# Performance work log

Measured on AMD Instinct MI355X. Metric: run time of the kernel, lower is better.

## Reference

```python
import jax, jax.numpy as jnp
import numpy as np
from jax.scipy.special import logsumexp

DIM_N, DIM_E, DIM_U = 64, 128, 64
MID, A = 32, 16
N_PER, B = 12, 128  # 128 fully-connected graphs of 12 nodes


def _lin_params(k, fin, fout):
    k1, k2 = jax.random.split(k)
    lim = 1.0 / np.sqrt(fin)
    W = jax.random.uniform(k1, (fin, fout), minval=-lim, maxval=lim)
    b = jax.random.uniform(k2, (fout,), minval=-lim, maxval=lim)
    return W, b


def setup_inputs() -> dict:
    key = jax.random.key(0)
    ks = jax.random.split(key, 12)
    # fully connected directed graph (no self loops), per component
    s, d = np.meshgrid(np.arange(N_PER), np.arange(N_PER), indexing='ij')
    m = s != d
    s1, d1 = s[m].astype(np.int64), d[m].astype(np.int64)
    Epg = s1.size  # 132
    M = np.zeros((N_PER, N_PER), np.int64)
    M[s1, d1] = np.arange(Epg)
    rev1 = M[d1, s1]
    noff = (np.arange(B, dtype=np.int64) * N_PER)[:, None]
    eoff = (np.arange(B, dtype=np.int64) * Epg)[:, None]
    src = jnp.asarray((s1[None] + noff).reshape(-1))
    dst = jnp.asarray((d1[None] + noff).reshape(-1))
    idx_revs = jnp.asarray((rev1[None] + eoff).reshape(-1))
    E, Nt = B * Epg, B * N_PER
    edge_feats = jax.random.normal(ks[0], (E, DIM_E))
    node_feats = jax.random.normal(ks[1], (Nt, DIM_N))
    graph_feats = jax.random.normal(ks[2], (B, DIM_U))
    edge_feat_reflected = edge_feats[idx_revs]
    u = jax.random.uniform(ks[3], (E, 2), minval=1e-6, maxval=1.0)
    gumbel_noise = -jnp.log(-jnp.log(u))
    W_jf, b_jf = _lin_params(ks[4], DIM_E + DIM_U, A * MID)
    W_if, b_if = _lin_params(ks[5], DIM_N + DIM_U, A)
    W_ju, b_ju = _lin_params(ks[6], DIM_E + DIM_U, A * MID)
    W_iu, b_iu = _lin_params(ks[7], DIM_N + DIM_U, A)
    W_fl, b_fl = _lin_params(ks[8], DIM_E + DIM_U, MID)
    W_cls, b_cls = _lin_params(ks[9], MID, 2)
    return dict(edge_feats=edge_feats, node_feats=node_feats, graph_feats=graph_feats,
                edge_feat_reflected=edge_feat_reflected, src=src, dst=dst, idx_revs=idx_revs,
                gumbel_noise=gumbel_noise, W_jf=W_jf, b_jf=b_jf, W_if=W_if, b_if=b_if,
                W_ju=W_ju, b_ju=b_ju, W_iu=W_iu, b_iu=b_iu, W_fl=W_fl, b_fl=b_fl,
                W_cls=W_cls, b_cls=b_cls)


def reference(edge_feats, node_feats, graph_feats, edge_feat_reflected, src, dst, idx_revs,
              gumbel_noise, W_jf, b_jf, W_if, b_if, W_ju, b_ju, W_iu, b_iu,
              W_fl, b_fl, W_cls, b_cls):
    Bn = graph_feats.shape[0]
    Nt = node_feats.shape[0]
    E = edge_feats.shape[0]
    npg = Nt // Bn          # nodes per graph == number of BP iterations
    epg = E // Bn
    a = b_if.shape[0]       # num_acts
    mid = W_cls.shape[0]    # mid_pair

    # broadcast graph-level features to edges / nodes
    u_e = jnp.repeat(graph_feats, epg, axis=0)   # [E, du]
    u_n = jnp.repeat(graph_feats, npg, axis=0)   # [Nt, du]

    xe = jnp.concatenate([edge_feats, u_e], axis=-1)
    xer = jnp.concatenate([edge_feat_reflected, u_e], axis=-1)
    xn = jnp.concatenate([node_feats, u_n], axis=-1)

    indiv_factor = xn @ W_if + b_if      # [Nt, A]
    indiv_util = xn @ W_iu + b_iu        # [Nt, A]

    fc = (xe @ W_jf + b_jf).reshape(E, a, mid)
    fcr = (xer @ W_jf + b_jf).reshape(E, a, mid)
    factor_vals = jnp.einsum('eam,ebm->eab', fc, fcr)   # [E, A, A]
    uc = (xe @ W_ju + b_ju).reshape(E, a, mid)
    ucr = (xer @ W_ju + b_ju).reshape(E, a, mid)
    util_vals = jnp.einsum('eam,ebm->eab', uc, ucr)     # [E, A, A]

    # hard gumbel-softmax edge gating; noise shared with reverse edge
    flag_repr = (xe @ W_fl + b_fl) * (xer @ W_fl + b_fl)
    logits = flag_repr @ W_cls + b_cls                  # [E, 2]
    eid = jnp.arange(E)
    noise = gumbel_noise[jnp.minimum(eid, idx_revs)]
    y_soft = jax.nn.softmax(logits + noise, axis=-1)
    y_hard = jax.nn.one_hot(jnp.argmax(y_soft, axis=-1), 2, dtype=y_soft.dtype)
    flags = y_soft + jax.lax.stop_gradient(y_hard - y_soft)
    flag0 = flags[:, 0][:, None]                        # [E, 1]

    fvT = factor_vals.transpose(0, 2, 1)
    uvT = util_vals.transpose(0, 2, 1)
    if_src, if_dst = indiv_factor[src], indiv_factor[dst]
    iu_src, iu_dst = indiv_util[src], indiv_util[dst]

    def step(carry, _):
        mm_n, um_n, msg_e, rmsg_e, umsg_e, rumsg_e = carry
        agg = mm_n[src] - rmsg_e + if_src                      # [E, A]
        m = factor_vals + agg[:, None, :]                      # [E, A, A]
        m_sum = jax.nn.log_softmax(logsumexp(m, axis=-1), axis=-1)
        new_msg = m_sum * flag0
        agg_rev = mm_n[dst] - msg_e + if_dst
        m_rev = fvT + agg_rev[:, None, :]
        m_rev_sum = jax.nn.log_softmax(logsumexp(m_rev, axis=-1), axis=-1)
        new_rmsg = m_rev_sum * flag0
        util = um_n[src] - rumsg_e + iu_src
        new_umsg = ((util_vals + util[:, None, :]) * jax.nn.softmax(m, axis=-1)).sum(-1) * flag0
        rev_util = um_n[dst] - umsg_e + iu_dst
        new_rumsg = ((uvT + rev_util[:, None, :]) * jax.nn.softmax(m_rev, axis=-1)).sum(-1) * flag0
        new_mm_n = jax.ops.segment_sum(new_msg, dst, num_segments=Nt)
        new_um_n = jax.ops.segment_sum(new_umsg, dst, num_segments=Nt)
        return (new_mm_n, new_um_n, new_msg, new_rmsg, new_umsg, new_rumsg), None

    zn = jnp.zeros((Nt, a), edge_feats.dtype)
    ze = jnp.zeros((E, a), edge_feats.dtype)
    carry0 = (zn, zn, ze, ze, ze, ze)
    (mm_n, um_n, _, _, _, _), _ = jax.lax.scan(step, carry0, None, length=npg)

    node0 = jnp.arange(Bn) * npg
    return (um_n + indiv_util)[node0]   # [B, A]
```

## Files before the change

kernel.cpp:

```cpp
#include <hip/hip_runtime.h>
#include <hip/hip_bf16.h>

typedef unsigned short ushort_t;
typedef __bf16 bf16x8 __attribute__((ext_vector_type(8)));
typedef float f32x4 __attribute__((ext_vector_type(4)));

#define E_TOT 16896
#define NT    1536
#define BGR   128
#define NPG   12
#define EPG   132
#define KD    192
#define KD2   576
#define NJ    512
#define NCAN  8448

#if defined(__has_builtin)
#  if __has_builtin(__builtin_amdgcn_global_load_lds)
#    define HAS_GLL 1
#  else
#    define HAS_GLL 0
#  endif
#else
#  define HAS_GLL 0
#endif

#if HAS_GLL
__device__ __forceinline__ void gll16(const ushort_t* g, ushort_t* s) {
    __builtin_amdgcn_global_load_lds(
        (const __attribute__((address_space(1))) unsigned int*)g,
        (__attribute__((address_space(3))) unsigned int*)s, 16, 0, 0);
}
#endif

__device__ __forceinline__ float b2f(ushort_t u) {
    union { float f; unsigned int i; } c; c.i = ((unsigned int)u) << 16; return c.f;
}
__device__ __forceinline__ ushort_t f2b(float f) {
    union { float f; unsigned int i; } c; c.f = f;
    unsigned int i = c.i;
    unsigned int r = (i + 0x7FFFu + ((i >> 16) & 1u)) >> 16;
    return (ushort_t)r;
}
__device__ __forceinline__ int rev_local(int i) {
    int s = i / 11;
    int p = i - 11 * s;
    int d = p + (p >= s ? 1 : 0);
    return d * 11 + (s < d ? s : s - 1);
}

__global__ __launch_bounds__(256) void prep_kernel(
    const float* __restrict__ Wjf, const float* __restrict__ Wju,
    const float* __restrict__ ef,  const float* __restrict__ gf,
    const float* __restrict__ nf,
    const float* __restrict__ Wif, const float* __restrict__ bif,
    const float* __restrict__ Wiu, const float* __restrict__ biu,
    ushort_t* __restrict__ WtJFs, ushort_t* __restrict__ WtJUs,
    ushort_t* __restrict__ XeS,
    float* __restrict__ IFF, float* __restrict__ IUU)
{
    __shared__ float Ws[128 * 32];
    __shared__ float xr[8][128];
    const int T1 = NJ * KD;
    const int NBE = (T1 + E_TOT * KD) / 256;
    if (blockIdx.x < (unsigned)NBE) {
        int idx = blockIdx.x * 256 + threadIdx.x;
        if (idx < T1) {
            int n = idx / KD, k = idx - n * KD;
            float wf = Wjf[k * NJ + n];
            ushort_t hf = f2b(wf);
            WtJFs[n * KD2 + k]       = hf;
            WtJFs[n * KD2 + 192 + k] = hf;
            WtJFs[n * KD2 + 384 + k] = f2b(wf - b2f(hf));
            float wu = Wju[k * NJ + n];
            ushort_t hu = f2b(wu);
            WtJUs[n * KD2 + k]       = hu;
            WtJUs[n * KD2 + 192 + k] = hu;
            WtJUs[n * KD2 + 384 + k] = f2b(wu - b2f(hu));
            return;
        }
        idx -= T1;
        int e = idx / KD, k = idx - e * KD;
        float x = (k < 128) ? ef[(size_t)e * 128 + k] : gf[(e / EPG) * 64 + (k - 128)];
        ushort_t h = f2b(x);
        XeS[(size_t)e * KD2 + k]       = h;
        XeS[(size_t)e * KD2 + 192 + k] = f2b(x - b2f(h));
        XeS[(size_t)e * KD2 + 384 + k] = h;
        return;
    }
    int tid = threadIdx.x;
    int n0 = (blockIdx.x - NBE) * 8;
    for (int i = tid; i < 128 * 32; i += 256) {
        int k = i >> 5, j = i & 31;
        Ws[i] = (j < 16) ? Wif[k * 16 + j] : Wiu[k * 16 + (j - 16)];
    }
    for (int i = tid; i < 8 * 128; i += 256) {
        int slot = i >> 7, k = i & 127;
        int n = n0 + slot;
        xr[slot][k] = (k < 64) ? nf[(size_t)n * 64 + k] : gf[(n / NPG) * 64 + (k - 64)];
    }
    __syncthreads();
    int slot = tid >> 5, j = tid & 31;
    float acc = (j < 16) ? bif[j] : biu[j - 16];
#pragma unroll 8
    for (int k = 0; k < 128; ++k) acc += xr[slot][k] * Ws[k * 32 + j];
    int n = n0 + slot;
    if (j < 16) IFF[n * 16 + j] = acc;
    else        IUU[n * 16 + (j - 16)] = acc;
}

__global__ __launch_bounds__(256) void gemm_kernel(
    const ushort_t* __restrict__ X,
    const ushort_t* __restrict__ Wt0, const ushort_t* __restrict__ Wt1,
    const float* __restrict__ b0, const float* __restrict__ b1,
    float* __restrict__ Hbase)
{
    __shared__ ushort_t As[2][128][32];
    __shared__ ushort_t Bs[2][2][128][32];
    int tid = threadIdx.x, lane = tid & 63, w = tid >> 6;
    int m0 = blockIdx.y * 128, n0 = blockIdx.x * 128;
    int wm = (w >> 1) * 64, wn = (w & 1) * 64;
    int r = lane & 15, q = lane >> 4;
    f32x4 acc[2][4][4] = {};

    int sr = w * 32 + (lane >> 2);
    int sc = (lane & 3) * 8;
    const ushort_t* xg0 = X   + (size_t)(m0 + sr)      * KD2 + sc;
    const ushort_t* xg1 = X   + (size_t)(m0 + sr + 16) * KD2 + sc;
    const ushort_t* w0g0 = Wt0 + (size_t)(n0 + sr)      * KD2 + sc;
    const ushort_t* w0g1 = Wt0 + (size_t)(n0 + sr + 16) * KD2 + sc;
    const ushort_t* w1g0 = Wt1 + (size_t)(n0 + sr)      * KD2 + sc;
    const ushort_t* w1g1 = Wt1 + (size_t)(n0 + sr + 16) * KD2 + sc;

#if HAS_GLL
    auto stage = [&](int p, int kk) {
        gll16(xg0 + kk,  &As[p][w * 32][0]);
        gll16(xg1 + kk,  &As[p][w * 32 + 16][0]);
        gll16(w0g0 + kk, &Bs[p][0][w * 32][0]);
        gll16(w0g1 + kk, &Bs[p][0][w * 32 + 16][0]);
        gll16(w1g0 + kk, &Bs[p][1][w * 32][0]);
        gll16(w1g1 + kk, &Bs[p][1][w * 32 + 16][0]);
    };
#else
    auto stage = [&](int p, int kk) {
        uint4 a0 = *(const uint4*)(xg0 + kk);
        uint4 a1 = *(const uint4*)(xg1 + kk);
        uint4 c0 = *(const uint4*)(w0g0 + kk);
        uint4 c1 = *(const uint4*)(w0g1 + kk);
        uint4 d0 = *(const uint4*)(w1g0 + kk);
        uint4 d1 = *(const uint4*)(w1g1 + kk);
        *(uint4*)&As[p][sr][sc]         = a0;
        *(uint4*)&As[p][sr + 16][sc]    = a1;
        *(uint4*)&Bs[p][0][sr][sc]      = c0;
        *(uint4*)&Bs[p][0][sr + 16][sc] = c1;
        *(uint4*)&Bs[p][1][sr][sc]      = d0;
        *(uint4*)&Bs[p][1][sr + 16][sc] = d1;
    };
#endif

    stage(0, 0);
    int cur = 0;
    for (int kk = 0; kk < KD2; kk += 32) {
        __syncthreads();
        if (kk + 32 < KD2) stage(cur ^ 1, kk + 32);
        bf16x8 af[4];
#pragma unroll
        for (int mi = 0; mi < 4; ++mi)
            af[mi] = *(const bf16x8*)&As[cur][wm + mi * 16 + r][q * 8];
#pragma unroll
        for (int z = 0; z < 2; ++z) {
            bf16x8 bf[4];
#pragma unroll
            for (int ni = 0; ni < 4; ++ni)
                bf[ni] = *(const bf16x8*)&Bs[cur][z][wn + ni * 16 + r][q * 8];
#pragma unroll
            for (int mi = 0; mi < 4; ++mi)
#pragma unroll
                for (int ni = 0; ni < 4; ++ni)
                    acc[z][mi][ni] = __builtin_amdgcn_mfma_f32_16x16x32_bf16(
                        af[mi], bf[ni], acc[z][mi][ni], 0, 0, 0);
        }
        cur ^= 1;
    }
#pragma unroll
    for (int z = 0; z < 2; ++z) {
        float* H = Hbase + (size_t)z * E_TOT * NJ;
        const float* bias = z ? b1 : b0;
#pragma unroll
        for (int ni = 0; ni < 4; ++ni) {
            int col = n0 + wn + ni * 16 + r;
            float bvf = bias[col];
#pragma unroll
            for (int mi = 0; mi < 4; ++mi) {
                int rowb = m0 + wm + mi * 16 + q * 4;
                float* dst = H + (size_t)rowb * NJ + col;
#pragma unroll
                for (int rr = 0; rr < 4; ++rr)
                    dst[(size_t)rr * NJ] = acc[z][mi][ni][rr] + bvf;
            }
        }
    }
}

__global__ __launch_bounds__(256) void pair_kernel(
    const float* __restrict__ Hbase, float* __restrict__ Obase)
{
    __shared__ float sA[4][16][36];
    __shared__ float sB[4][16][36];
    __shared__ float sC[4][16][20];
    const float* H = Hbase + (size_t)blockIdx.y * E_TOT * NJ;
    float* OutV = Obase + (size_t)blockIdx.y * E_TOT * 256;
    int tid = threadIdx.x, w = tid >> 6, lane = tid & 63;
    int c = blockIdx.x * 4 + w;
    int gg = c / 66, cl = c - gg * 66;
    int s = 0;
    while (cl >= 11 - s) { cl -= 11 - s; ++s; }
    int d = s + 1 + cl;
    int e  = gg * EPG + s * 11 + (d - 1);
    int re = gg * EPG + d * 11 + s;
    const float* hA = H + (size_t)e * NJ;
    const float* hB = H + (size_t)re * NJ;
    int a = lane >> 2, mseg = (lane & 3) * 8;
    float4 va0 = *(const float4*)(hA + a * 32 + mseg);
    float4 va1 = *(const float4*)(hA + a * 32 + mseg + 4);
    float4 vb0 = *(const float4*)(hB + a * 32 + mseg);
    float4 vb1 = *(const float4*)(hB + a * 32 + mseg + 4);
    *(float4*)&sA[w][a][mseg]     = va0;
    *(float4*)&sA[w][a][mseg + 4] = va1;
    *(float4*)&sB[w][a][mseg]     = vb0;
    *(float4*)&sB[w][a][mseg + 4] = vb1;
    __syncthreads();

    int b = lane & 15, a0 = (lane >> 4) * 4;
    float4 ac0 = {0,0,0,0}, ac1 = {0,0,0,0}, ac2 = {0,0,0,0}, ac3 = {0,0,0,0};
#pragma unroll
    for (int m4 = 0; m4 < 8; ++m4) {
        float4 vb = *(const float4*)&sB[w][b][m4 * 4];
        float4 x0 = *(const float4*)&sA[w][a0 + 0][m4 * 4];
        float4 x1 = *(const float4*)&sA[w][a0 + 1][m4 * 4];
        float4 x2 = *(const float4*)&sA[w][a0 + 2][m4 * 4];
        float4 x3 = *(const float4*)&sA[w][a0 + 3][m4 * 4];
        ac0.x += x0.x * vb.x; ac0.y += x0.y * vb.y; ac0.z += x0.z * vb.z; ac0.w += x0.w * vb.w;
        ac1.x += x1.x * vb.x; ac1.y += x1.y * vb.y; ac1.z += x1.z * vb.z; ac1.w += x1.w * vb.w;
        ac2.x += x2.x * vb.x; ac2.y += x2.y * vb.y; ac2.z += x2.z * vb.z; ac2.w += x2.w * vb.w;
        ac3.x += x3.x * vb.x; ac3.y += x3.y * vb.y; ac3.z += x3.z * vb.z; ac3.w += x3.w * vb.w;
    }
    float v0 = ac0.x + ac0.y + ac0.z + ac0.w;
    float v1 = ac1.x + ac1.y + ac1.z + ac1.w;
    float v2 = ac2.x + ac2.y + ac2.z + ac2.w;
    float v3 = ac3.x + ac3.y + ac3.z + ac3.w;
    float* oe = OutV + (size_t)e * 256;
    oe[(a0 + 0) * 16 + b] = v0;
    oe[(a0 + 1) * 16 + b] = v1;
    oe[(a0 + 2) * 16 + b] = v2;
    oe[(a0 + 3) * 16 + b] = v3;
    sC[w][b][a0 + 0] = v0;
    sC[w][b][a0 + 1] = v1;
    sC[w][b][a0 + 2] = v2;
    sC[w][b][a0 + 3] = v3;
    __syncthreads();
    int rr = lane >> 2, cc = (lane & 3) * 4;
    float4 t4 = { sC[w][rr][cc], sC[w][rr][cc + 1], sC[w][rr][cc + 2], sC[w][rr][cc + 3] };
    *(float4*)(OutV + (size_t)re * 256 + lane * 4) = t4;
}

__global__ __launch_bounds__(256) void hfl_kernel(
    const float* __restrict__ ef, const float* __restrict__ gf,
    const float* __restrict__ Wfl, const float* __restrict__ bfl,
    float* __restrict__ HFL)
{
    __shared__ float Ws[KD][32];
    __shared__ float xr[64][KD];
    int tid = threadIdx.x;
    int e0 = blockIdx.x * 64;
    for (int i = tid; i < KD * 32; i += 256) Ws[i >> 5][i & 31] = Wfl[i];
    for (int i4 = tid; i4 < 64 * 48; i4 += 256) {
        int slot = i4 / 48, kq = i4 - slot * 48;
        int e = e0 + slot;
        float4 v;
        if (kq < 32) v = *(const float4*)&ef[(size_t)e * 128 + kq * 4];
        else         v = *(const float4*)&gf[(e / EPG) * 64 + (kq - 32) * 4];
        *(float4*)&xr[slot][kq * 4] = v;
    }
    __syncthreads();
    int j = tid & 31, es = tid >> 5;
    float acc[8];
#pragma unroll
    for (int i = 0; i < 8; ++i) acc[i] = bfl[j];
    for (int k = 0; k < KD; k += 4) {
        float w0 = Ws[k][j], w1 = Ws[k + 1][j], w2 = Ws[k + 2][j], w3 = Ws[k + 3][j];
#pragma unroll
        for (int i = 0; i < 8; ++i) {
            float4 x4 = *(const float4*)&xr[es + 8 * i][k];
            acc[i] += x4.x * w0; acc[i] += x4.y * w1;
            acc[i] += x4.z * w2; acc[i] += x4.w * w3;
        }
    }
#pragma unroll
    for (int i = 0; i < 8; ++i)
        HFL[(size_t)(e0 + es + 8 * i) * 32 + j] = acc[i];
}

__global__ __launch_bounds__(704, 3) void bp_kernel(
    const float* __restrict__ FV, const float* __restrict__ UV,
    const float* __restrict__ HFL, const float* __restrict__ Wcls,
    const float* __restrict__ bcls, const float* __restrict__ gum,
    const float* __restrict__ IFF, const float* __restrict__ IUU,
    float* __restrict__ out)
{
    int g = blockIdx.x, tid = threadIdx.x;
    __shared__ float msg[2][EPG][16];
    __shared__ float umsg[2][EPG][16];
    __shared__ float Asum[NPG][16], Usum[NPG][16];
    __shared__ float iffs[NPG][16], iuus[NPG][16];
    __shared__ float fls[EPG];

    for (int i = tid; i < 2 * EPG * 16; i += 704) {
        (&msg[0][0][0])[i] = 0.f;
        (&umsg[0][0][0])[i] = 0.f;
    }
    if (tid < NPG * 16) {
        float fi = IFF[g * NPG * 16 + tid];
        float ui = IUU[g * NPG * 16 + tid];
        (&iffs[0][0])[tid] = fi; (&iuus[0][0])[tid] = ui;
        (&Asum[0][0])[tid] = fi; (&Usum[0][0])[tid] = ui;
    }
    if (tid < EPG) {
        int el = tid, rel = rev_local(el);
        int e = g * EPG + el, re = g * EPG + rel;
        float l0 = bcls[0], l1 = bcls[1];
        const float* ha = HFL + (size_t)e * 32;
        const float* hb = HFL + (size_t)re * 32;
#pragma unroll
        for (int j = 0; j < 32; ++j) {
            float pp = ha[j] * hb[j];
            l0 += pp * Wcls[j * 2 + 0];
            l1 += pp * Wcls[j * 2 + 1];
        }
        int mn = min(e, re);
        l0 += gum[(size_t)mn * 2 + 0];
        l1 += gum[(size_t)mn * 2 + 1];
        fls[el] = (l0 >= l1) ? 1.0f : 0.0f;
    }

    int w44 = tid >> 4, a = tid & 15;
    int sidx[3], ridx[3], eidx[3];
    float fv[3][16], uv[3][16], fle[3];
    const float* fvg = FV + (size_t)g * EPG * 256;
    const float* uvg = UV + (size_t)g * EPG * 256;
#pragma unroll
    for (int j = 0; j < 3; ++j) {
        int e = j * 44 + w44;
        eidx[j] = e;
        sidx[j] = e / 11;
        ridx[j] = rev_local(e);
        const float* fr = fvg + (size_t)e * 256 + a * 16;
        const float* ur = uvg + (size_t)e * 256 + a * 16;
#pragma unroll
        for (int qq = 0; qq < 4; ++qq) {
            float4 f4 = *(const float4*)(fr + qq * 4);
            float4 u4 = *(const float4*)(ur + qq * 4);
            fv[j][qq * 4 + 0] = f4.x; fv[j][qq * 4 + 1] = f4.y;
            fv[j][qq * 4 + 2] = f4.z; fv[j][qq * 4 + 3] = f4.w;
            uv[j][qq * 4 + 0] = u4.x; uv[j][qq * 4 + 1] = u4.y;
            uv[j][qq * 4 + 2] = u4.z; uv[j][qq * 4 + 3] = u4.w;
        }
    }
    __syncthreads();
#pragma unroll
    for (int j = 0; j < 3; ++j) fle[j] = fls[eidx[j]];

    int cur = 0;
    for (int it = 0; it < NPG; ++it) {
        int nxt = cur ^ 1;
#pragma unroll
        for (int j = 0; j < 3; ++j) {
            int e = eidx[j], s = sidx[j], re = ridx[j];
            float t_m[16], t_u[16];
#pragma unroll
            for (int qq = 0; qq < 4; ++qq) {
                float4 av  = *(const float4*)&Asum[s][qq * 4];
                float4 mv  = *(const float4*)&msg[cur][re][qq * 4];
                float4 usv = *(const float4*)&Usum[s][qq * 4];
                float4 umv = *(const float4*)&umsg[cur][re][qq * 4];
                t_m[qq * 4 + 0] = fv[j][qq * 4 + 0] + (av.x - mv.x);
                t_m[qq * 4 + 1] = fv[j][qq * 4 + 1] + (av.y - mv.y);
                t_m[qq * 4 + 2] = fv[j][qq * 4 + 2] + (av.z - mv.z);
                t_m[qq * 4 + 3] = fv[j][qq * 4 + 3] + (av.w - mv.w);
                t_u[qq * 4 + 0] = uv[j][qq * 4 + 0] + (usv.x - umv.x);
                t_u[qq * 4 + 1] = uv[j][qq * 4 + 1] + (usv.y - umv.y);
                t_u[qq * 4 + 2] = uv[j][qq * 4 + 2] + (usv.z - umv.z);
                t_u[qq * 4 + 3] = uv[j][qq * 4 + 3] + (usv.w - umv.w);
            }
            float mx = t_m[0];
#pragma unroll
            for (int b = 1; b < 16; ++b) mx = fmaxf(mx, t_m[b]);
            float S = 0.f, num = 0.f;
#pragma unroll
            for (int b = 0; b < 16; ++b) {
                float ev = __expf(t_m[b] - mx);
                S += ev;
                num += t_u[b] * ev;
            }
            float lse = mx + __logf(S);
            float unv = num / S;
            float M2 = lse;
            M2 = fmaxf(M2, __shfl_xor(M2, 1));
            M2 = fmaxf(M2, __shfl_xor(M2, 2));
            M2 = fmaxf(M2, __shfl_xor(M2, 4));
            M2 = fmaxf(M2, __shfl_xor(M2, 8));
            float se = __expf(lse - M2);
            se += __shfl_xor(se, 1);
            se += __shfl_xor(se, 2);
            se += __shfl_xor(se, 4);
            se += __shfl_xor(se, 8);
            float LSE = M2 + __logf(se);
            msg[nxt][e][a] = (lse - LSE) * fle[j];
            umsg[nxt][e][a] = unv * fle[j];
        }
        __syncthreads();
        if (tid < NPG * 16) {
            int n = tid >> 4, aa = tid & 15;
            float sm = 0.f, su = 0.f;
#pragma unroll
            for (int s = 0; s < NPG; ++s) {
                if (s == n) continue;
                int le = s * 11 + (n < s ? n : n - 1);
                sm += msg[nxt][le][aa];
                su += umsg[nxt][le][aa];
            }
            Asum[n][aa] = sm + iffs[n][aa];
            Usum[n][aa] = su + iuus[n][aa];
        }
        __syncthreads();
        cur = nxt;
    }
    if (tid < 16) {
        out[g * 16 + tid] = Usum[0][tid];
    }
}

extern "C" void kernel_launch(void* const* d_in, const int* in_sizes, int n_in,
                              void* d_out, int out_size, void* d_ws, size_t ws_size,
                              hipStream_t stream) {
    const float* edge_feats  = (const float*)d_in[0];
    const float* node_feats  = (const float*)d_in[1];
    const float* graph_feats = (const float*)d_in[2];
    const float* gumbel      = (const float*)d_in[7];
    const float* W_jf        = (const float*)d_in[8];
    const float* b_jf        = (const float*)d_in[9];
    const float* W_if        = (const float*)d_in[10];
    const float* b_if        = (const float*)d_in[11];
    const float* W_ju        = (const float*)d_in[12];
    const float* b_ju        = (const float*)d_in[13];
    const float* W_iu        = (const float*)d_in[14];
    const float* b_iu        = (const float*)d_in[15];
    const float* W_fl        = (const float*)d_in[16];
    const float* b_fl        = (const float*)d_in[17];
    const float* W_cls       = (const float*)d_in[18];
    const float* b_cls       = (const float*)d_in[19];
    float* out = (float*)d_out;
    (void)in_sizes; (void)n_in; (void)out_size; (void)ws_size;

    size_t off = 0;
    char* base = (char*)d_ws;
    auto alloc = [&](size_t bytes) {
        void* p = base + off;
        off += (bytes + 255) & ~(size_t)255;
        return p;
    };
    ushort_t* XeS   = (ushort_t*)alloc((size_t)E_TOT * KD2 * 2);
    ushort_t* WtJFs = (ushort_t*)alloc((size_t)NJ * KD2 * 2);
    ushort_t* WtJUs = (ushort_t*)alloc((size_t)NJ * KD2 * 2);
    float*    HFL   = (float*)   alloc((size_t)E_TOT * 32 * 4);
    float*    IFFp  = (float*)   alloc((size_t)NT * 16 * 4);
    float*    IUUp  = (float*)   alloc((size_t)NT * 16 * 4);
    float*    H2    = (float*)   alloc((size_t)E_TOT * NJ * 2 * 4);
    float*    FVUV  = (float*)   alloc((size_t)E_TOT * 512 * 4);
    float* FVv = FVUV;
    float* UVv = FVUV + (size_t)E_TOT * 256;

    const int NBE = (NJ * KD + E_TOT * KD) / 256;
    const int prep_blocks = NBE + NT / 8;

    prep_kernel<<<prep_blocks, 256, 0, stream>>>(
        W_jf, W_ju, edge_feats, graph_feats, node_feats,
        W_if, b_if, W_iu, b_iu, WtJFs, WtJUs, XeS, IFFp, IUUp);
    hfl_kernel<<<E_TOT / 64, 256, 0, stream>>>(edge_feats, graph_feats, W_fl, b_fl, HFL);
    gemm_kernel<<<dim3(NJ / 128, E_TOT / 128), 256, 0, stream>>>(
        XeS, WtJFs, WtJUs, b_jf, b_ju, H2);
    pair_kernel<<<dim3(NCAN / 4, 2), 256, 0, stream>>>(H2, FVUV);
    bp_kernel<<<BGR, 704, 0, stream>>>(FVv, UVv, HFL, W_cls, b_cls, gumbel,
                                       IFFp, IUUp, out);
}
```

Measured before the change: 241.5 us.

## Hoist per-graph feature projection out of edge GEMM into precomputed bias

The graph-feature part of the concatenated edge input is the same for all 132 edges of a graph, so its projection (plus the bias) is computed once per graph in the prep kernel and added in the GEMM epilogue. This cuts the GEMM K dimension from 576 to 384 and shrinks the prepared input buffer. The GEMM is also split across a z grid dimension with one weight matrix per block, which halves the accumulators and LDS per block and doubles the block count. In exchange the epilogue reads a per-graph bias table with an integer division per row, and the graph-feature term is now computed in fp32 rather than split-bf16.

```diff
diff --git a/kernel.cpp b/kernel.cpp
--- a/kernel.cpp
+++ b/kernel.cpp
@@ -11,7 +11,8 @@
 #define NPG   12
 #define EPG   132
 #define KD    192
-#define KD2   576
+#define KDE   128
+#define KD2   384
 #define NJ    512
 #define NCAN  8448
 
@@ -52,44 +53,59 @@
 __global__ __launch_bounds__(256) void prep_kernel(
     const float* __restrict__ Wjf, const float* __restrict__ Wju,
     const float* __restrict__ ef,  const float* __restrict__ gf,
+    const float* __restrict__ bjf, const float* __restrict__ bju,
     const float* __restrict__ nf,
     const float* __restrict__ Wif, const float* __restrict__ bif,
     const float* __restrict__ Wiu, const float* __restrict__ biu,
     ushort_t* __restrict__ WtJFs, ushort_t* __restrict__ WtJUs,
-    ushort_t* __restrict__ XeS,
+    ushort_t* __restrict__ XeS, float* __restrict__ CG,
     float* __restrict__ IFF, float* __restrict__ IUU)
 {
     __shared__ float Ws[128 * 32];
     __shared__ float xr[8][128];
-    const int T1 = NJ * KD;
-    const int NBE = (T1 + E_TOT * KD) / 256;
+    const int T1 = NJ * KDE;
+    const int NBE = (T1 + E_TOT * KDE) / 256;
     if (blockIdx.x < (unsigned)NBE) {
         int idx = blockIdx.x * 256 + threadIdx.x;
         if (idx < T1) {
-            int n = idx / KD, k = idx - n * KD;
+            int n = idx / KDE, k = idx - n * KDE;
             float wf = Wjf[k * NJ + n];
             ushort_t hf = f2b(wf);
             WtJFs[n * KD2 + k]       = hf;
-            WtJFs[n * KD2 + 192 + k] = hf;
-            WtJFs[n * KD2 + 384 + k] = f2b(wf - b2f(hf));
+            WtJFs[n * KD2 + 128 + k] = hf;
+            WtJFs[n * KD2 + 256 + k] = f2b(wf - b2f(hf));
             float wu = Wju[k * NJ + n];
             ushort_t hu = f2b(wu);
             WtJUs[n * KD2 + k]       = hu;
-            WtJUs[n * KD2 + 192 + k] = hu;
-            WtJUs[n * KD2 + 384 + k] = f2b(wu - b2f(hu));
+            WtJUs[n * KD2 + 128 + k] = hu;
+            WtJUs[n * KD2 + 256 + k] = f2b(wu - b2f(hu));
             return;
         }
         idx -= T1;
-        int e = idx / KD, k = idx - e * KD;
-        float x = (k < 128) ? ef[(size_t)e * 128 + k] : gf[(e / EPG) * 64 + (k - 128)];
+        int e = idx / KDE, k = idx - e * KDE;
+        float x = ef[(size_t)e * KDE + k];
         ushort_t h = f2b(x);
         XeS[(size_t)e * KD2 + k]       = h;
-        XeS[(size_t)e * KD2 + 192 + k] = f2b(x - b2f(h));
-        XeS[(size_t)e * KD2 + 384 + k] = h;
+        XeS[(size_t)e * KD2 + 128 + k] = f2b(x - b2f(h));
+        XeS[(size_t)e * KD2 + 256 + k] = h;
         return;
     }
+    if (blockIdx.x < (unsigned)(NBE + 512)) {
+        int cidx = (blockIdx.x - NBE) * 256 + threadIdx.x;
+        int z = cidx >> 16;
+        int rem = cidx & 65535;
+        int g = rem >> 9, n = rem & 511;
+        const float* W = z ? Wju : Wjf;
+        float acc = (z ? bju : bjf)[n];
+        const float* gr = gf + g * 64;
+#pragma unroll 8
+        for (int k = 0; k < 64; ++k)
+            acc += gr[k] * W[(size_t)(128 + k) * NJ + n];
+        CG[cidx] = acc;
+        return;
+    }
     int tid = threadIdx.x;
-    int n0 = (blockIdx.x - NBE) * 8;
+    int n0 = (blockIdx.x - NBE - 512) * 8;
     for (int i = tid; i < 128 * 32; i += 256) {
         int k = i >> 5, j = i & 31;
         Ws[i] = (j < 16) ? Wif[k * 16 + j] : Wiu[k * 16 + (j - 16)];
@@ -112,49 +128,45 @@
 __global__ __launch_bounds__(256) void gemm_kernel(
     const ushort_t* __restrict__ X,
     const ushort_t* __restrict__ Wt0, const ushort_t* __restrict__ Wt1,
-    const float* __restrict__ b0, const float* __restrict__ b1,
-    float* __restrict__ Hbase)
+    const float* __restrict__ CG, float* __restrict__ Hbase)
 {
     __shared__ ushort_t As[2][128][32];
-    __shared__ ushort_t Bs[2][2][128][32];
+    __shared__ ushort_t Bs[2][128][32];
+    int z = blockIdx.z;
+    const ushort_t* Wt = z ? Wt1 : Wt0;
+    const float* cgz = CG + (size_t)z * 128 * NJ;
+    float* H = Hbase + (size_t)z * E_TOT * NJ;
+
     int tid = threadIdx.x, lane = tid & 63, w = tid >> 6;
     int m0 = blockIdx.y * 128, n0 = blockIdx.x * 128;
     int wm = (w >> 1) * 64, wn = (w & 1) * 64;
     int r = lane & 15, q = lane >> 4;
-    f32x4 acc[2][4][4] = {};
+    f32x4 acc[4][4] = {};
 
     int sr = w * 32 + (lane >> 2);
     int sc = (lane & 3) * 8;
-    const ushort_t* xg0 = X   + (size_t)(m0 + sr)      * KD2 + sc;
-    const ushort_t* xg1 = X   + (size_t)(m0 + sr + 16) * KD2 + sc;
-    const ushort_t* w0g0 = Wt0 + (size_t)(n0 + sr)      * KD2 + sc;
-    const ushort_t* w0g1 = Wt0 + (size_t)(n0 + sr + 16) * KD2 + sc;
-    const ushort_t* w1g0 = Wt1 + (size_t)(n0 + sr)      * KD2 + sc;
-    const ushort_t* w1g1 = Wt1 + (size_t)(n0 + sr + 16) * KD2 + sc;
+    const ushort_t* xg0 = X  + (size_t)(m0 + sr)      * KD2 + sc;
+    const ushort_t* xg1 = X  + (size_t)(m0 + sr + 16) * KD2 + sc;
+    const ushort_t* wg0 = Wt + (size_t)(n0 + sr)      * KD2 + sc;
+    const ushort_t* wg1 = Wt + (size_t)(n0 + sr + 16) * KD2 + sc;
 
 #if HAS_GLL
     auto stage = [&](int p, int kk) {
-        gll16(xg0 + kk,  &As[p][w * 32][0]);
-        gll16(xg1 + kk,  &As[p][w * 32 + 16][0]);
-        gll16(w0g0 + kk, &Bs[p][0][w * 32][0]);
-        gll16(w0g1 + kk, &Bs[p][0][w * 32 + 16][0]);
-        gll16(w1g0 + kk, &Bs[p][1][w * 32][0]);
-        gll16(w1g1 + kk, &Bs[p][1][w * 32 + 16][0]);
+        gll16(xg0 + kk, &As[p][w * 32][0]);
+        gll16(xg1 + kk, &As[p][w * 32 + 16][0]);
+        gll16(wg0 + kk, &Bs[p][w * 32][0]);
+        gll16(wg1 + kk, &Bs[p][w * 32 + 16][0]);
     };
 #else
     auto stage = [&](int p, int kk) {
         uint4 a0 = *(const uint4*)(xg0 + kk);
         uint4 a1 = *(const uint4*)(xg1 + kk);
-        uint4 c0 = *(const uint4*)(w0g0 + kk);
-        uint4 c1 = *(const uint4*)(w0g1 + kk);
-        uint4 d0 = *(const uint4*)(w1g0 + kk);
-        uint4 d1 = *(const uint4*)(w1g1 + kk);
-        *(uint4*)&As[p][sr][sc]         = a0;
-        *(uint4*)&As[p][sr + 16][sc]    = a1;
-        *(uint4*)&Bs[p][0][sr][sc]      = c0;
-        *(uint4*)&Bs[p][0][sr + 16][sc] = c1;
-        *(uint4*)&Bs[p][1][sr][sc]      = d0;
-        *(uint4*)&Bs[p][1][sr + 16][sc] = d1;
+        uint4 b0 = *(const uint4*)(wg0 + kk);
+        uint4 b1 = *(const uint4*)(wg1 + kk);
+        *(uint4*)&As[p][sr][sc]      = a0;
+        *(uint4*)&As[p][sr + 16][sc] = a1;
+        *(uint4*)&Bs[p][sr][sc]      = b0;
+        *(uint4*)&Bs[p][sr + 16][sc] = b1;
     };
 #endif
 
@@ -163,40 +175,32 @@
     for (int kk = 0; kk < KD2; kk += 32) {
         __syncthreads();
         if (kk + 32 < KD2) stage(cur ^ 1, kk + 32);
-        bf16x8 af[4];
+        bf16x8 af[4], bf[4];
 #pragma unroll
         for (int mi = 0; mi < 4; ++mi)
             af[mi] = *(const bf16x8*)&As[cur][wm + mi * 16 + r][q * 8];
 #pragma unroll
-        for (int z = 0; z < 2; ++z) {
-            bf16x8 bf[4];
+        for (int ni = 0; ni < 4; ++ni)
+            bf[ni] = *(const bf16x8*)&Bs[cur][wn + ni * 16 + r][q * 8];
+#pragma unroll
+        for (int mi = 0; mi < 4; ++mi)
 #pragma unroll
             for (int ni = 0; ni < 4; ++ni)
-                bf[ni] = *(const bf16x8*)&Bs[cur][z][wn + ni * 16 + r][q * 8];
-#pragma unroll
-            for (int mi = 0; mi < 4; ++mi)
-#pragma unroll
-                for (int ni = 0; ni < 4; ++ni)
-                    acc[z][mi][ni] = __builtin_amdgcn_mfma_f32_16x16x32_bf16(
-                        af[mi], bf[ni], acc[z][mi][ni], 0, 0, 0);
-        }
+                acc[mi][ni] = __builtin_amdgcn_mfma_f32_16x16x32_bf16(
+                    af[mi], bf[ni], acc[mi][ni], 0, 0, 0);
         cur ^= 1;
     }
 #pragma unroll
-    for (int z = 0; z < 2; ++z) {
-        float* H = Hbase + (size_t)z * E_TOT * NJ;
-        const float* bias = z ? b1 : b0;
-#pragma unroll
-        for (int ni = 0; ni < 4; ++ni) {
-            int col = n0 + wn + ni * 16 + r;
-            float bvf = bias[col];
-#pragma unroll
-            for (int mi = 0; mi < 4; ++mi) {
-                int rowb = m0 + wm + mi * 16 + q * 4;
-                float* dst = H + (size_t)rowb * NJ + col;
-#pragma unroll
-                for (int rr = 0; rr < 4; ++rr)
-                    dst[(size_t)rr * NJ] = acc[z][mi][ni][rr] + bvf;
+    for (int ni = 0; ni < 4; ++ni) {
+        int col = n0 + wn + ni * 16 + r;
+#pragma unroll
+        for (int mi = 0; mi < 4; ++mi) {
+            int rowb = m0 + wm + mi * 16 + q * 4;
+            float* dst = H + (size_t)rowb * NJ + col;
+#pragma unroll
+            for (int rr = 0; rr < 4; ++rr) {
+                int gg = (rowb + rr) / EPG;
+                dst[(size_t)rr * NJ] = acc[mi][ni][rr] + cgz[(size_t)gg * NJ + col];
             }
         }
     }
@@ -472,6 +476,7 @@
     ushort_t* XeS   = (ushort_t*)alloc((size_t)E_TOT * KD2 * 2);
     ushort_t* WtJFs = (ushort_t*)alloc((size_t)NJ * KD2 * 2);
     ushort_t* WtJUs = (ushort_t*)alloc((size_t)NJ * KD2 * 2);
+    float*    CGp   = (float*)   alloc((size_t)2 * 128 * NJ * 4);
     float*    HFL   = (float*)   alloc((size_t)E_TOT * 32 * 4);
     float*    IFFp  = (float*)   alloc((size_t)NT * 16 * 4);
     float*    IUUp  = (float*)   alloc((size_t)NT * 16 * 4);
@@ -480,15 +485,15 @@
     float* FVv = FVUV;
     float* UVv = FVUV + (size_t)E_TOT * 256;
 
-    const int NBE = (NJ * KD + E_TOT * KD) / 256;
-    const int prep_blocks = NBE + NT / 8;
+    const int NBE = (NJ * KDE + E_TOT * KDE) / 256;
+    const int prep_blocks = NBE + 512 + NT / 8;
 
     prep_kernel<<<prep_blocks, 256, 0, stream>>>(
-        W_jf, W_ju, edge_feats, graph_feats, node_feats,
-        W_if, b_if, W_iu, b_iu, WtJFs, WtJUs, XeS, IFFp, IUUp);
+        W_jf, W_ju, edge_feats, graph_feats, b_jf, b_ju, node_feats,
+        W_if, b_if, W_iu, b_iu, WtJFs, WtJUs, XeS, CGp, IFFp, IUUp);
     hfl_kernel<<<E_TOT / 64, 256, 0, stream>>>(edge_feats, graph_feats, W_fl, b_fl, HFL);
-    gemm_kernel<<<dim3(NJ / 128, E_TOT / 128), 256, 0, stream>>>(
-        XeS, WtJFs, WtJUs, b_jf, b_ju, H2);
+    gemm_kernel<<<dim3(NJ / 128, E_TOT / 128, 2), 256, 0, stream>>>(
+        XeS, WtJFs, WtJUs, CGp, H2);
     pair_kernel<<<dim3(NCAN / 4, 2), 256, 0, stream>>>(H2, FVUV);
     bp_kernel<<<BGR, 704, 0, stream>>>(FVv, UVv, HFL, W_cls, b_cls, gumbel,
                                        IFFp, IUUp, out);
```

Result: faster. 236.5 us (-2.1%).
